# Kernel optimization log

Hardware: AMD Instinct MI355X
Metric: run time of the kernel (lower is better)

## Reference

```python
import jax, jax.numpy as jnp
import numpy as np

N_QUBITS = 4
N_LAYERS = 2


def _apply_rx(state, theta, wire):
    """Apply RX(theta) on `wire`. state: [B] + [2]*n complex. theta: [B] or scalar."""
    n = state.ndim - 1
    ax = wire + 1
    half = jnp.asarray(theta) * 0.5
    c = jnp.cos(half)
    s = jnp.sin(half)
    # broadcast angle over the remaining qubit axes after taking the wire slice
    c = jnp.reshape(c, c.shape + (1,) * (n - 1))
    s = jnp.reshape(s, s.shape + (1,) * (n - 1))
    s0 = jnp.take(state, 0, axis=ax)
    s1 = jnp.take(state, 1, axis=ax)
    new0 = c * s0 - 1j * s * s1
    new1 = -1j * s * s0 + c * s1
    return jnp.stack([new0, new1], axis=ax)


def _apply_cnot(state, control, target):
    cax = control + 1
    tax = target + 1
    sub0 = jnp.take(state, 0, axis=cax)
    sub1 = jnp.take(state, 1, axis=cax)
    tax_sub = tax if tax < cax else tax - 1
    sub1 = jnp.flip(sub1, axis=tax_sub)  # X on target when control == 1
    return jnp.stack([sub0, sub1], axis=cax)


def _quantum_circuit(x, w):
    """AngleEmbedding(RX) + BasicEntanglerLayers(RX + CNOT ring), PauliZ expvals.
    x: [B, n_qubits] float32 angles; w: [n_layers, n_qubits] float32.
    Returns [B, n_qubits] float32."""
    B = x.shape[0]
    n = N_QUBITS
    state = jnp.zeros((B,) + (2,) * n, dtype=jnp.complex64)
    state = state.at[(slice(None),) + (0,) * n].set(1.0)
    # AngleEmbedding: RX(x_q) on wire q (per-sample angles)
    for q in range(n):
        state = _apply_rx(state, x[:, q], q)
    # BasicEntanglerLayers: per layer, RX(w[l,q]) on each wire then CNOT ring
    for l in range(N_LAYERS):
        for q in range(n):
            state = _apply_rx(state, w[l, q], q)
        for q in range(n):
            state = _apply_cnot(state, q, (q + 1) % n)
    probs = jnp.abs(state) ** 2  # [B, 2,2,2,2]
    flat = probs.reshape(B, -1)  # [B, 16]
    # <Z_q> = sum_b p(b) * (+1 if bit q == 0 else -1)
    bits = ((jnp.arange(2 ** n)[:, None] >> (n - 1 - jnp.arange(n))[None, :]) & 1)
    signs = (1.0 - 2.0 * bits).astype(jnp.float32)  # [16, n]
    return flat @ signs  # [B, n]


def setup_inputs() -> dict:
    key = jax.random.key(0)
    ks = jax.random.split(key, 5)
    B = 65536
    inputs = jax.random.normal(ks[0], (B, 28, 28), dtype=jnp.float32)
    W1 = jax.random.normal(ks[1], (784, N_QUBITS), dtype=jnp.float32) * 0.05
    b1 = jnp.zeros((N_QUBITS,), dtype=jnp.float32)
    qw = jax.random.normal(ks[2], (N_LAYERS, N_QUBITS), dtype=jnp.float32) * 0.1
    W2 = jax.random.normal(ks[3], (N_QUBITS, 32), dtype=jnp.float32) * 0.3
    b2 = jnp.zeros((32,), dtype=jnp.float32)
    W3 = jax.random.normal(ks[4], (32, 2), dtype=jnp.float32) * 0.2
    b3 = jnp.zeros((2,), dtype=jnp.float32)
    return {"inputs": inputs, "W1": W1, "b1": b1, "qw": qw, "W2": W2, "b2": b2, "W3": W3, "b3": b3}


def reference(inputs, W1, b1, qw, W2, b2, W3, b3):
    B = inputs.shape[0]
    flat = inputs.reshape(B, -1)                      # flatten
    pre = jax.nn.relu(flat @ W1 + b1)                 # dense_preprocess [B, 4]
    q = _quantum_circuit(pre, qw)                     # [B, 4]
    q = jnp.where(jnp.isnan(q), jnp.zeros_like(q), q)
    post = jax.nn.relu(q @ W2 + b2)                   # dense_postprocess [B, 32]
    return jax.nn.softmax(post @ W3 + b3, axis=-1)    # output_layer [B, 2]
```

## Files before the change

kernel.cpp:

```cpp
#include <hip/hip_runtime.h>
#include <math.h>


constexpr int ROW  = 784;
constexpr int ROW4 = 196;

__device__ __forceinline__ void apply_rx(float (&sr)[16], float (&si)[16],
                                         int mask, float c, float s)
{
    #pragma unroll
    for (int i = 0; i < 16; i++) {
        if (!(i & mask)) {
            int j = i | mask;
            float x0 = sr[i], y0 = si[i], x1 = sr[j], y1 = si[j];
            sr[i] = fmaf(c, x0,  s * y1);
            si[i] = fmaf(c, y0, -s * x1);
            sr[j] = fmaf(c, x1,  s * y0);
            si[j] = fmaf(c, y1, -s * x0);
        }
    }
}

__device__ __forceinline__ void apply_cnot(float (&sr)[16], float (&si)[16],
                                           int cmask, int tmask)
{
    #pragma unroll
    for (int i = 0; i < 16; i++) {
        if ((i & cmask) && !(i & tmask)) {
            int j = i | tmask;
            float tr = sr[i]; sr[i] = sr[j]; sr[j] = tr;
            float ti = si[i]; si[i] = si[j]; si[j] = ti;
        }
    }
}

#define FMA_ONE(xv, wrow, o0) \
    a[(o0)+0] = fmaf(xv, wrow.x, a[(o0)+0]); \
    a[(o0)+1] = fmaf(xv, wrow.y, a[(o0)+1]); \
    a[(o0)+2] = fmaf(xv, wrow.z, a[(o0)+2]); \
    a[(o0)+3] = fmaf(xv, wrow.w, a[(o0)+3]);

#define FMA_ROUND(xb, o0, o1) { \
    _Pragma("unroll") \
    for (int i = 0; i < 4; i++) { \
        FMA_ONE(xb[i].x,     w[i][0], o0) FMA_ONE(xb[4+i].x, w[i][0], o1) \
        FMA_ONE(xb[i].y,     w[i][1], o0) FMA_ONE(xb[4+i].y, w[i][1], o1) \
        FMA_ONE(xb[i].z,     w[i][2], o0) FMA_ONE(xb[4+i].z, w[i][2], o1) \
        FMA_ONE(xb[i].w,     w[i][3], o0) FMA_ONE(xb[4+i].w, w[i][3], o1) \
    } }

#define LOAD_ROUND(dst, sA, sB) { \
    const float4* p0_ = X4 + (size_t)(sA) * ROW4; \
    const float4* p1_ = X4 + (size_t)(sB) * ROW4; \
    dst[0] = p0_[lane];        dst[4] = p1_[lane]; \
    dst[1] = p0_[lane + 64];   dst[5] = p1_[lane + 64]; \
    dst[2] = p0_[lane + 128];  dst[6] = p1_[lane + 128]; \
    dst[3] = tail ? p0_[192 + lane] : zero4; \
    dst[7] = tail ? p1_[192 + lane] : zero4; }

#define CLMP(v) (((v) < sl) ? (v) : sl)

__global__ __launch_bounds__(256) void fused_kernel(
    const float* __restrict__ X,
    const float* __restrict__ W1,
    const float* __restrict__ b1,
    const float* __restrict__ qw,
    const float* __restrict__ W2,
    const float* __restrict__ b2,
    const float* __restrict__ W3,
    const float* __restrict__ b3,
    float* __restrict__ out,
    int B)
{
    const int lane = threadIdx.x & 63;
    const int wid  = (blockIdx.x * 256 + threadIdx.x) >> 6;
    const bool tail = (lane < 4);
    const int  jt   = 192 + (lane & 3);

    const float4* X4   = reinterpret_cast<const float4*>(X);
    const float4* W1f4 = reinterpret_cast<const float4*>(W1);

    float4 w[4][4];
    #pragma unroll
    for (int i = 0; i < 4; i++) {
        const int j4 = (i < 3) ? (lane + (i << 6)) : jt;
        #pragma unroll
        for (int p = 0; p < 4; p++) w[i][p] = W1f4[4 * j4 + p];
    }

    const int idx = ((lane >> 5) & 1) * 16 + ((lane >> 4) & 1) * 8 +
                    ((lane >> 3) & 1) * 4  + ((lane >> 2) & 1) * 2 +
                    ((lane >> 1) & 1);
    const float bl = b1[idx & 3];

    const bool b5  = (lane & 32) != 0;
    const bool b4  = (lane & 16) != 0;
    const bool b3f = (lane & 8)  != 0;
    const bool b2f = (lane & 4)  != 0;
    const bool b1f = (lane & 2)  != 0;

    const float4 zero4 = make_float4(0.f, 0.f, 0.f, 0.f);
    const int sl = B - 1;

    const int S = wid * 32;
    if (S >= B) return;

    float p0 = 0.f, p1 = 0.f, p2 = 0.f, p3 = 0.f;

    float4 xA[8], xB[8];
    LOAD_ROUND(xA, CLMP(S),     CLMP(S + 1))
    LOAD_ROUND(xB, CLMP(S + 2), CLMP(S + 3))

    #pragma unroll
    for (int it = 0; it < 4; it++) {
        const int Sb = S + it * 8;

        float a[32];
        #pragma unroll
        for (int i = 0; i < 32; i++) a[i] = 0.f;

        FMA_ROUND(xA, 0, 4)
        LOAD_ROUND(xA, CLMP(Sb + 4), CLMP(Sb + 5))
        FMA_ROUND(xB, 8, 12)
        LOAD_ROUND(xB, CLMP(Sb + 6), CLMP(Sb + 7))
        FMA_ROUND(xA, 16, 20)
        if (it < 3) LOAD_ROUND(xA, CLMP(Sb + 8), CLMP(Sb + 9))
        FMA_ROUND(xB, 24, 28)
        if (it < 3) LOAD_ROUND(xB, CLMP(Sb + 10), CLMP(Sb + 11))

        float v16[16];
        #pragma unroll
        for (int i = 0; i < 16; i++) {
            float kv = b5 ? a[i + 16] : a[i];
            float sv = b5 ? a[i]      : a[i + 16];
            v16[i] = kv + __shfl_xor(sv, 32);
        }
        float v8a[8];
        #pragma unroll
        for (int i = 0; i < 8; i++) {
            float kv = b4 ? v16[i + 8] : v16[i];
            float sv = b4 ? v16[i]     : v16[i + 8];
            v8a[i] = kv + __shfl_xor(sv, 16);
        }
        float v4a[4];
        #pragma unroll
        for (int i = 0; i < 4; i++) {
            float kv = b3f ? v8a[i + 4] : v8a[i];
            float sv = b3f ? v8a[i]     : v8a[i + 4];
            v4a[i] = kv + __shfl_xor(sv, 8);
        }
        float v2a[2];
        #pragma unroll
        for (int i = 0; i < 2; i++) {
            float kv = b2f ? v4a[i + 2] : v4a[i];
            float sv = b2f ? v4a[i]     : v4a[i + 2];
            v2a[i] = kv + __shfl_xor(sv, 4);
        }
        float kv = b1f ? v2a[1] : v2a[0];
        float sv = b1f ? v2a[0] : v2a[1];
        float v1 = kv + __shfl_xor(sv, 2);
        v1 += __shfl_xor(v1, 1);

        const float pre_val = fmaxf(v1 + bl, 0.f);

        const float g0 = __shfl(pre_val, ((lane & 7) << 3) + 0);
        const float g1 = __shfl(pre_val, ((lane & 7) << 3) + 2);
        const float g2 = __shfl(pre_val, ((lane & 7) << 3) + 4);
        const float g3 = __shfl(pre_val, ((lane & 7) << 3) + 6);
        if ((lane >> 3) == it) { p0 = g0; p1 = g1; p2 = g2; p3 = g3; }
    }

    if (lane < 32 && S + lane < B) {
        const int s = S + lane;

        float sr[16], si[16];
        #pragma unroll
        for (int i = 0; i < 16; i++) { sr[i] = 0.f; si[i] = 0.f; }
        sr[0] = 1.f;

        {
            float c, sn;
            __sincosf(p0 * 0.5f, &sn, &c); apply_rx(sr, si, 8, c, sn);
            __sincosf(p1 * 0.5f, &sn, &c); apply_rx(sr, si, 4, c, sn);
            __sincosf(p2 * 0.5f, &sn, &c); apply_rx(sr, si, 2, c, sn);
            __sincosf(p3 * 0.5f, &sn, &c); apply_rx(sr, si, 1, c, sn);
        }

        #pragma unroll
        for (int l = 0; l < 2; l++) {
            #pragma unroll
            for (int q = 0; q < 4; q++) {
                float c, sn;
                __sincosf(qw[l * 4 + q] * 0.5f, &sn, &c);
                apply_rx(sr, si, 8 >> q, c, sn);
            }
            apply_cnot(sr, si, 8, 4);
            apply_cnot(sr, si, 4, 2);
            apply_cnot(sr, si, 2, 1);
            apply_cnot(sr, si, 1, 8);
        }

        float z0 = 0.f, z1 = 0.f, z2 = 0.f, z3 = 0.f;
        #pragma unroll
        for (int i = 0; i < 16; i++) {
            float p = fmaf(sr[i], sr[i], si[i] * si[i]);
            z0 += (i & 8) ? -p : p;
            z1 += (i & 4) ? -p : p;
            z2 += (i & 2) ? -p : p;
            z3 += (i & 1) ? -p : p;
        }
        z0 = (z0 == z0) ? z0 : 0.f;
        z1 = (z1 == z1) ? z1 : 0.f;
        z2 = (z2 == z2) ? z2 : 0.f;
        z3 = (z3 == z3) ? z3 : 0.f;

        float l0 = b3[0], l1 = b3[1];
        #pragma unroll
        for (int k = 0; k < 32; k++) {
            float v = b2[k];
            v = fmaf(z0, W2[k],      v);
            v = fmaf(z1, W2[32 + k], v);
            v = fmaf(z2, W2[64 + k], v);
            v = fmaf(z3, W2[96 + k], v);
            v = fmaxf(v, 0.f);
            l0 = fmaf(v, W3[2 * k],     l0);
            l1 = fmaf(v, W3[2 * k + 1], l1);
        }

        float m  = fmaxf(l0, l1);
        float e0 = __expf(l0 - m), e1 = __expf(l1 - m);
        float inv = 1.f / (e0 + e1);
        reinterpret_cast<float2*>(out)[s] = make_float2(e0 * inv, e1 * inv);
    }
}

extern "C" void kernel_launch(void* const* d_in, const int* in_sizes, int n_in,
                              void* d_out, int out_size, void* d_ws, size_t ws_size,
                              hipStream_t stream)
{
    const float* X  = (const float*)d_in[0];
    const float* W1 = (const float*)d_in[1];
    const float* b1 = (const float*)d_in[2];
    const float* qw = (const float*)d_in[3];
    const float* W2 = (const float*)d_in[4];
    const float* b2 = (const float*)d_in[5];
    const float* W3 = (const float*)d_in[6];
    const float* b3 = (const float*)d_in[7];

    const int B = in_sizes[0] / ROW;

    const int blocks = (B + 127) / 128;
    fused_kernel<<<blocks, 256, 0, stream>>>(X, W1, b1, qw, W2, b2, W3, b3,
                                             (float*)d_out, B);
}
```

Baseline: 294.4 us.

## Halve samples per wave, use contiguous per-lane column chunks, shorten reduction tree

Each wave now handles 16 samples instead of 32, processing two samples per iteration with only 8 accumulators, so fewer registers are live. Each lane loads four consecutive float4 columns of a row instead of strided ones, and lanes past 49 get zero weights. The cross-lane reduction now starts from 8 partial sums, and launch_bounds asks for 4 blocks per CU to raise occupancy. The grid doubles in size. Lanes 49-63 now do wasted loads and FMAs, and each wave has less memory-level parallelism.

```diff
diff --git a/kernel.cpp b/kernel.cpp
--- a/kernel.cpp
+++ b/kernel.cpp
@@ -40,27 +40,24 @@
     a[(o0)+2] = fmaf(xv, wrow.z, a[(o0)+2]); \
     a[(o0)+3] = fmaf(xv, wrow.w, a[(o0)+3]);
 
-#define FMA_ROUND(xb, o0, o1) { \
+#define FMA2(xb) { \
     _Pragma("unroll") \
     for (int i = 0; i < 4; i++) { \
-        FMA_ONE(xb[i].x,     w[i][0], o0) FMA_ONE(xb[4+i].x, w[i][0], o1) \
-        FMA_ONE(xb[i].y,     w[i][1], o0) FMA_ONE(xb[4+i].y, w[i][1], o1) \
-        FMA_ONE(xb[i].z,     w[i][2], o0) FMA_ONE(xb[4+i].z, w[i][2], o1) \
-        FMA_ONE(xb[i].w,     w[i][3], o0) FMA_ONE(xb[4+i].w, w[i][3], o1) \
+        FMA_ONE(xb[i].x, w[i][0], 0) FMA_ONE(xb[4+i].x, w[i][0], 4) \
+        FMA_ONE(xb[i].y, w[i][1], 0) FMA_ONE(xb[4+i].y, w[i][1], 4) \
+        FMA_ONE(xb[i].z, w[i][2], 0) FMA_ONE(xb[4+i].z, w[i][2], 4) \
+        FMA_ONE(xb[i].w, w[i][3], 0) FMA_ONE(xb[4+i].w, w[i][3], 4) \
     } }
 
-#define LOAD_ROUND(dst, sA, sB) { \
-    const float4* p0_ = X4 + (size_t)(sA) * ROW4; \
-    const float4* p1_ = X4 + (size_t)(sB) * ROW4; \
-    dst[0] = p0_[lane];        dst[4] = p1_[lane]; \
-    dst[1] = p0_[lane + 64];   dst[5] = p1_[lane + 64]; \
-    dst[2] = p0_[lane + 128];  dst[6] = p1_[lane + 128]; \
-    dst[3] = tail ? p0_[192 + lane] : zero4; \
-    dst[7] = tail ? p1_[192 + lane] : zero4; }
-
 #define CLMP(v) (((v) < sl) ? (v) : sl)
 
-__global__ __launch_bounds__(256) void fused_kernel(
+#define LOAD2(dst, sA, sB) { \
+    const float4* rA_ = X4 + (size_t)CLMP(sA) * ROW4; \
+    const float4* rB_ = X4 + (size_t)CLMP(sB) * ROW4; \
+    dst[0] = rA_[c0]; dst[1] = rA_[c1]; dst[2] = rA_[c2]; dst[3] = rA_[c3]; \
+    dst[4] = rB_[c0]; dst[5] = rB_[c1]; dst[6] = rB_[c2]; dst[7] = rB_[c3]; }
+
+__global__ __launch_bounds__(256, 4) void fused_kernel(
     const float* __restrict__ X,
     const float* __restrict__ W1,
     const float* __restrict__ b1,
@@ -74,103 +71,90 @@
 {
     const int lane = threadIdx.x & 63;
     const int wid  = (blockIdx.x * 256 + threadIdx.x) >> 6;
-    const bool tail = (lane < 4);
-    const int  jt   = 192 + (lane & 3);
 
     const float4* X4   = reinterpret_cast<const float4*>(X);
     const float4* W1f4 = reinterpret_cast<const float4*>(W1);
 
+    const int c0 = (4 * lane     < ROW4) ? 4 * lane     : ROW4 - 1;
+    const int c1 = (4 * lane + 1 < ROW4) ? 4 * lane + 1 : ROW4 - 1;
+    const int c2 = (4 * lane + 2 < ROW4) ? 4 * lane + 2 : ROW4 - 1;
+    const int c3 = (4 * lane + 3 < ROW4) ? 4 * lane + 3 : ROW4 - 1;
+
+    const bool wok = (lane < 49);
+    const float4 zero4 = make_float4(0.f, 0.f, 0.f, 0.f);
     float4 w[4][4];
     #pragma unroll
     for (int i = 0; i < 4; i++) {
-        const int j4 = (i < 3) ? (lane + (i << 6)) : jt;
-        #pragma unroll
-        for (int p = 0; p < 4; p++) w[i][p] = W1f4[4 * j4 + p];
-    }
-
-    const int idx = ((lane >> 5) & 1) * 16 + ((lane >> 4) & 1) * 8 +
-                    ((lane >> 3) & 1) * 4  + ((lane >> 2) & 1) * 2 +
-                    ((lane >> 1) & 1);
-    const float bl = b1[idx & 3];
+        #pragma unroll
+        for (int c = 0; c < 4; c++) {
+            float4 t = W1f4[wok ? (16 * lane + 4 * i + c) : 0];
+            w[i][c] = wok ? t : zero4;
+        }
+    }
+
+    const float bl = b1[(lane >> 3) & 3];
 
     const bool b5  = (lane & 32) != 0;
     const bool b4  = (lane & 16) != 0;
     const bool b3f = (lane & 8)  != 0;
-    const bool b2f = (lane & 4)  != 0;
-    const bool b1f = (lane & 2)  != 0;
-
-    const float4 zero4 = make_float4(0.f, 0.f, 0.f, 0.f);
+
     const int sl = B - 1;
 
-    const int S = wid * 32;
+    const int S = wid * 16;
     if (S >= B) return;
 
     float p0 = 0.f, p1 = 0.f, p2 = 0.f, p3 = 0.f;
 
     float4 xA[8], xB[8];
-    LOAD_ROUND(xA, CLMP(S),     CLMP(S + 1))
-    LOAD_ROUND(xB, CLMP(S + 2), CLMP(S + 3))
-
-    #pragma unroll
-    for (int it = 0; it < 4; it++) {
-        const int Sb = S + it * 8;
-
-        float a[32];
-        #pragma unroll
-        for (int i = 0; i < 32; i++) a[i] = 0.f;
-
-        FMA_ROUND(xA, 0, 4)
-        LOAD_ROUND(xA, CLMP(Sb + 4), CLMP(Sb + 5))
-        FMA_ROUND(xB, 8, 12)
-        LOAD_ROUND(xB, CLMP(Sb + 6), CLMP(Sb + 7))
-        FMA_ROUND(xA, 16, 20)
-        if (it < 3) LOAD_ROUND(xA, CLMP(Sb + 8), CLMP(Sb + 9))
-        FMA_ROUND(xB, 24, 28)
-        if (it < 3) LOAD_ROUND(xB, CLMP(Sb + 10), CLMP(Sb + 11))
-
-        float v16[16];
-        #pragma unroll
-        for (int i = 0; i < 16; i++) {
-            float kv = b5 ? a[i + 16] : a[i];
-            float sv = b5 ? a[i]      : a[i + 16];
-            v16[i] = kv + __shfl_xor(sv, 32);
-        }
-        float v8a[8];
-        #pragma unroll
-        for (int i = 0; i < 8; i++) {
-            float kv = b4 ? v16[i + 8] : v16[i];
-            float sv = b4 ? v16[i]     : v16[i + 8];
-            v8a[i] = kv + __shfl_xor(sv, 16);
-        }
-        float v4a[4];
+    LOAD2(xA, S,     S + 1)
+    LOAD2(xB, S + 2, S + 3)
+
+    #pragma unroll
+    for (int it = 0; it < 8; it++) {
+        float4 (&xb)[8] = (it & 1) ? xB : xA;
+
+        float a[8];
+        #pragma unroll
+        for (int i = 0; i < 8; i++) a[i] = 0.f;
+
+        FMA2(xb)
+        if (it < 6) {
+            const int Sn = S + (it + 2) * 2;
+            if (it & 1) { LOAD2(xB, Sn, Sn + 1) }
+            else        { LOAD2(xA, Sn, Sn + 1) }
+        }
+
+        float v4[4];
         #pragma unroll
         for (int i = 0; i < 4; i++) {
-            float kv = b3f ? v8a[i + 4] : v8a[i];
-            float sv = b3f ? v8a[i]     : v8a[i + 4];
-            v4a[i] = kv + __shfl_xor(sv, 8);
-        }
-        float v2a[2];
+            float kv = b5 ? a[i + 4] : a[i];
+            float sv = b5 ? a[i]     : a[i + 4];
+            v4[i] = kv + __shfl_xor(sv, 32);
+        }
+        float v2[2];
         #pragma unroll
         for (int i = 0; i < 2; i++) {
-            float kv = b2f ? v4a[i + 2] : v4a[i];
-            float sv = b2f ? v4a[i]     : v4a[i + 2];
-            v2a[i] = kv + __shfl_xor(sv, 4);
-        }
-        float kv = b1f ? v2a[1] : v2a[0];
-        float sv = b1f ? v2a[0] : v2a[1];
-        float v1 = kv + __shfl_xor(sv, 2);
+            float kv = b4 ? v4[i + 2] : v4[i];
+            float sv = b4 ? v4[i]     : v4[i + 2];
+            v2[i] = kv + __shfl_xor(sv, 16);
+        }
+        float kv = b3f ? v2[1] : v2[0];
+        float sv = b3f ? v2[0] : v2[1];
+        float v1 = kv + __shfl_xor(sv, 8);
+        v1 += __shfl_xor(v1, 4);
+        v1 += __shfl_xor(v1, 2);
         v1 += __shfl_xor(v1, 1);
 
         const float pre_val = fmaxf(v1 + bl, 0.f);
 
-        const float g0 = __shfl(pre_val, ((lane & 7) << 3) + 0);
-        const float g1 = __shfl(pre_val, ((lane & 7) << 3) + 2);
-        const float g2 = __shfl(pre_val, ((lane & 7) << 3) + 4);
-        const float g3 = __shfl(pre_val, ((lane & 7) << 3) + 6);
-        if ((lane >> 3) == it) { p0 = g0; p1 = g1; p2 = g2; p3 = g3; }
-    }
-
-    if (lane < 32 && S + lane < B) {
+        const float g0 = __shfl(pre_val, ((lane & 1) << 5) + 0);
+        const float g1 = __shfl(pre_val, ((lane & 1) << 5) + 8);
+        const float g2 = __shfl(pre_val, ((lane & 1) << 5) + 16);
+        const float g3 = __shfl(pre_val, ((lane & 1) << 5) + 24);
+        if ((lane >> 1) == it) { p0 = g0; p1 = g1; p2 = g2; p3 = g3; }
+    }
+
+    if (lane < 16 && S + lane < B) {
         const int s = S + lane;
 
         float sr[16], si[16];
@@ -249,7 +233,7 @@
 
     const int B = in_sizes[0] / ROW;
 
-    const int blocks = (B + 127) / 128;
+    const int blocks = (B + 63) / 64;
     fused_kernel<<<blocks, 256, 0, stream>>>(X, W1, b1, qw, W2, b2, W3, b3,
                                              (float*)d_out, B);
 }
```

Result: slower. 330.8 us (+12.4%).
